# Optimization experiments

Measured on AMD Instinct MI355X. Metric: run time of the kernel, lower is better.

The kernel has to match this reference:

```python
import jax, jax.numpy as jnp
import numpy as np


def _softmax_bmm(sjt, x):
    # sjt: [b, m, n] scores; softmax over n, then weighted sum of x [b, n, d]
    a = jax.nn.softmax(sjt, axis=2)
    return jnp.einsum('bmn,bnd->bmd', a, x)


def concat_att(x, y, Wc1, Wc2, vc):
    s1 = x @ Wc1  # [b, n, h]
    s2 = y @ Wc2  # [b, m, h]
    sjt = jnp.tanh(s1[:, None, :, :] + s2[:, :, None, :]) @ vc  # [b, m, n]
    return _softmax_bmm(sjt, x)


def dot_att(x, y, Wd, vd):
    # torch: vd(tanh(Wd(x_n * y_m))) ; (x_n*y_m)@Wd == einsum over feature dim
    s = jnp.einsum('bnd,bmd,dh->bmnh', x, y, Wd)  # [b, m, n, h]
    sjt = jnp.tanh(s) @ vd  # [b, m, n]
    return _softmax_bmm(sjt, x)


def minus_att(x, y, Wm, vm):
    # (x_n - y_m)@Wm == x@Wm broadcast-minus y@Wm
    sx = x @ Wm  # [b, n, h]
    sy = y @ Wm  # [b, m, h]
    sjt = jnp.tanh(sx[:, None, :, :] - sy[:, :, None, :]) @ vm  # [b, m, n]
    return _softmax_bmm(sjt, x)


def bilinear_att(x, y, Wb):
    sjt = jnp.einsum('bmd,bnd->bmn', y, x @ Wb)
    return _softmax_bmm(sjt, x)


def setup_inputs() -> dict:
    H = 128          # hidden_size
    D = 2 * H        # encoder feature dim (2*hidden)
    B, N, M = 4, 256, 256
    key = jax.random.key(0)
    ks = jax.random.split(key, 12)
    sD = 1.0 / np.sqrt(D)
    sH = 1.0 / np.sqrt(H)
    return {
        'x0_enc': jax.random.normal(ks[0], (B, N, D), jnp.float32),
        'x1_enc': jax.random.normal(ks[1], (B, M, D), jnp.float32),
        'Wc1': jax.random.normal(ks[2], (D, H), jnp.float32) * sD,
        'Wc2': jax.random.normal(ks[3], (D, H), jnp.float32) * sD,
        'vc': jax.random.normal(ks[4], (H,), jnp.float32) * sH,
        'Wb': jax.random.normal(ks[5], (D, D), jnp.float32) * sD,
        'Wd1': jax.random.normal(ks[6], (D, H), jnp.float32) * sD,
        'vd1': jax.random.normal(ks[7], (H,), jnp.float32) * sH,
        'Wd2': jax.random.normal(ks[8], (D, H), jnp.float32) * sD,
        'vd2': jax.random.normal(ks[9], (H,), jnp.float32) * sH,
        'Wm': jax.random.normal(ks[10], (D, H), jnp.float32) * sD,
        'vm': jax.random.normal(ks[11], (H,), jnp.float32) * sH,
    }


def reference(x0_enc, x1_enc, Wc1, Wc2, vc, Wb, Wd1, vd1, Wd2, vd2, Wm, vm):
    # attention_type == 'all'
    qtc = concat_att(x0_enc, x1_enc, Wc1, Wc2, vc)   # [b, m, d]
    qtb = bilinear_att(x0_enc, x1_enc, Wb)           # [b, m, d]
    qts = dot_att(x0_enc, x1_enc, Wd1, vd1)          # [b, m, d]
    qtd = dot_att(x1_enc, x0_enc, Wd2, vd2)          # [b, n, d] (n == m)
    qtm = minus_att(x0_enc, x1_enc, Wm, vm)          # [b, m, d]
    stacked = jnp.stack([x1_enc, qts, qtc, qtd, qtb, qtm], axis=0)
    return jnp.max(stacked, axis=0)
```

## Files before the change

kernel.cpp:

```cpp
#include <hip/hip_runtime.h>
#include <math.h>

typedef short short8 __attribute__((ext_vector_type(8)));
typedef float f32x4 __attribute__((ext_vector_type(4)));
typedef unsigned short US;

#if __has_builtin(__builtin_amdgcn_exp2f)
#define EXP2(x) __builtin_amdgcn_exp2f(x)
#else
#define EXP2(x) exp2f(x)
#endif
#define RCP(x) __builtin_amdgcn_rcpf(x)

#define C2 2.8853900817779268f

__device__ __forceinline__ float bf2f(US u) {
    return __uint_as_float(((unsigned int)u) << 16);
}
__device__ __forceinline__ US f2bf(float f) {
    unsigned int x = __float_as_uint(f);
    return (US)((x + 0x7FFFu + ((x >> 16) & 1u)) >> 16);
}
__device__ __forceinline__ US f2bf_fast(float f) {
    return (US)((__float_as_uint(f) + 0x8000u) >> 16);
}


__global__ void prep_kernel(const float* __restrict__ x0, const float* __restrict__ x1,
                            const float* __restrict__ Wc1, const float* __restrict__ Wc2,
                            const float* __restrict__ Wm, const float* __restrict__ Wd1,
                            const float* __restrict__ Wd2, const float* __restrict__ Wb,
                            US* __restrict__ x0b, US* __restrict__ x1b,
                            US* __restrict__ x0lo, US* __restrict__ x1lo,
                            US* __restrict__ WcT1, US* __restrict__ WcT2,
                            US* __restrict__ WmT, US* __restrict__ WdT1, US* __restrict__ WdT2,
                            US* __restrict__ WbThi, US* __restrict__ WbTlo,
                            US* __restrict__ x0T, US* __restrict__ x1T) {
    const int id = blockIdx.x;
    const int t = threadIdx.x;
    if (id < 512) {
        const int tensor = id >> 8;
        const float* src = tensor ? x1 : x0;
        US* dhi = tensor ? x1b : x0b;
        US* dlo = tensor ? x1lo : x0lo;
        const int idx = (id & 255) * 256 + t;
        float4 v = ((const float4*)src)[idx];
        float f[4] = {v.x, v.y, v.z, v.w};
        ushort4 hi, lo;
        US* hp = (US*)&hi;
        US* lp = (US*)&lo;
        #pragma unroll
        for (int j = 0; j < 4; ++j) {
            US h = f2bf(f[j]);
            hp[j] = h;
            lp[j] = f2bf(f[j] - bf2f(h));
        }
        ((ushort4*)dhi)[idx] = hi;
        ((ushort4*)dlo)[idx] = lo;
    } else if (id < 1152) {
        const int j = id - 512;
        const int mat = j >> 7;
        const float* src = (mat == 0) ? Wc1 : (mat == 1) ? Wc2 : (mat == 2) ? Wm : (mat == 3) ? Wd1 : Wd2;
        US* dst = (mat == 0) ? WcT1 : (mat == 1) ? WcT2 : (mat == 2) ? WmT : (mat == 3) ? WdT1 : WdT2;
        const int el = (j & 127) * 256 + t;
        const int d = el >> 7, h = el & 127;
        dst[h * 256 + d] = f2bf(src[d * 128 + h]);
    } else if (id < 1408) {
        const int j = id - 1152;
        const int el = j * 256 + t;
        const int d = el >> 8, dp = el & 255;
        float v = Wb[d * 256 + dp];
        US h = f2bf(v);
        WbThi[dp * 256 + d] = h;
        WbTlo[dp * 256 + d] = f2bf(v - bf2f(h));
    } else {
        const int j = id - 1408;
        const int tensor = j >> 9;
        const int j2 = j & 511;
        const int b = j2 >> 7;
        const int dp = j2 & 127;
        const float* src = tensor ? x1 : x0;
        US* dst = tensor ? x1T : x0T;
        float2 v = *(const float2*)(src + (size_t)(b * 256 + t) * 256 + dp * 2);
        dst[(size_t)(b * 256 + dp * 2) * 256 + t] = f2bf(v.x);
        dst[(size_t)(b * 256 + dp * 2 + 1) * 256 + t] = f2bf(v.y);
    }
}

__global__ __launch_bounds__(512, 4)
void combo_kernel(const US* __restrict__ x0b, const US* __restrict__ x0lo,
                  const US* __restrict__ x1b,
                  const US* __restrict__ WcT1, const US* __restrict__ WcT2,
                  const US* __restrict__ WmT,
                  const US* __restrict__ WbThi, const US* __restrict__ WbTlo,
                  const US* __restrict__ WdT1, const US* __restrict__ WdT2,
                  const float* __restrict__ x0, const float* __restrict__ x1,
                  const float* __restrict__ vd1, const float* __restrict__ vd2,
                  US* __restrict__ S1T, US* __restrict__ SXT,
                  float* __restrict__ S2, float* __restrict__ SY,
                  US* __restrict__ XBhi, US* __restrict__ XBlo,
                  float* __restrict__ sjt_s, float* __restrict__ sjt_d) {
    __shared__ __align__(16) US Wp[128 * 256];
    const int bid = blockIdx.x;
    const int t = threadIdx.x;
    const int lane = t & 63;
    const int w = t >> 6;
    const int arow = lane & 15;
    const int kgrp = lane >> 4;

    if (bid < 192) {
        if (w >= 4) return;
        const int id = bid;
        const int rg = id & 15;
        const int t2 = id >> 4;
        const int b = t2 / 3;
        const int which = t2 - b * 3;

        const US* A = (which == 2 ? x1b : x0b) + (size_t)(b * 256 + rg * 16 + arow) * 256 + kgrp * 8;
        const US* Alo = x0lo + (size_t)(b * 256 + rg * 16 + arow) * 256 + kgrp * 8;

        const f32x4 vzero = {0.f, 0.f, 0.f, 0.f};
        f32x4 acc[4];
        #pragma unroll
        for (int cj = 0; cj < 4; ++cj) acc[cj] = vzero;

        if (which == 1) {
            #pragma unroll
            for (int kk = 0; kk < 8; ++kk) {
                short8 ahi = *(const short8*)(A + kk * 32);
                short8 alo = *(const short8*)(Alo + kk * 32);
                #pragma unroll
                for (int cj = 0; cj < 4; ++cj) {
                    const int ct = w * 4 + cj;
                    short8 bhi = *(const short8*)(WbThi + (ct * 16 + arow) * 256 + kk * 32 + kgrp * 8);
                    short8 blo = *(const short8*)(WbTlo + (ct * 16 + arow) * 256 + kk * 32 + kgrp * 8);
                    acc[cj] = __builtin_amdgcn_mfma_f32_16x16x32_bf16(ahi, bhi, acc[cj], 0, 0, 0);
                    acc[cj] = __builtin_amdgcn_mfma_f32_16x16x32_bf16(ahi, blo, acc[cj], 0, 0, 0);
                    acc[cj] = __builtin_amdgcn_mfma_f32_16x16x32_bf16(alo, bhi, acc[cj], 0, 0, 0);
                }
            }
            #pragma unroll
            for (int cj = 0; cj < 4; ++cj) {
                const int ct = w * 4 + cj;
                #pragma unroll
                for (int r = 0; r < 4; ++r) {
                    const int n = rg * 16 + kgrp * 4 + r;
                    const int dp = ct * 16 + arow;
                    float val = acc[cj][r];
                    US h = f2bf(val);
                    US l = f2bf(val - bf2f(h));
                    XBhi[(size_t)(b * 256 + n) * 256 + dp] = h;
                    XBlo[(size_t)(b * 256 + n) * 256 + dp] = l;
                }
            }
        } else {
            const US* WA = (which == 0) ? WcT1 : WcT2;
            #pragma unroll
            for (int kk = 0; kk < 8; ++kk) {
                short8 a = *(const short8*)(A + kk * 32);
                #pragma unroll
                for (int cj = 0; cj < 4; ++cj) {
                    const int ct = w * 4 + cj;
                    const US* brow = (ct < 8) ? (WA + (ct * 16 + arow) * 256)
                                              : (WmT + ((ct - 8) * 16 + arow) * 256);
                    short8 bf = *(const short8*)(brow + kk * 32 + kgrp * 8);
                    acc[cj] = __builtin_amdgcn_mfma_f32_16x16x32_bf16(a, bf, acc[cj], 0, 0, 0);
                }
            }
            #pragma unroll
            for (int cj = 0; cj < 4; ++cj) {
                const int ct = w * 4 + cj;
                #pragma unroll
                for (int r = 0; r < 4; ++r) {
                    const int row = rg * 16 + kgrp * 4 + r;
                    const int h = (ct < 8) ? ct * 16 + arow : (ct - 8) * 16 + arow;
                    float val = acc[cj][r];
                    if (which == 0) {
                        US* dst = (ct < 8) ? S1T : SXT;
                        dst[(size_t)(b * 256 + row) * 128 + h] = f2bf(val);
                    } else {
                        float* dst = (ct < 8) ? S2 : SY;
                        dst[(size_t)(b * 256 + row) * 128 + h] = val;
                    }
                }
            }
        }
        return;
    }

    const int id2 = bid - 192;
    const int m    = id2 & 255;
    const int b    = (id2 >> 8) & 3;
    const int mech = id2 >> 10;
    const US* xA = (mech == 0 ? x0b : x1b) + (size_t)b * 65536;
    const float* yrow = (mech == 0 ? x1 : x0) + (size_t)(b * 256 + m) * 256;
    const US* WT = (mech == 0 ? WdT1 : WdT2);
    const float* v = (mech == 0 ? vd1 : vd2);
    float* out = (mech == 0 ? sjt_s : sjt_d) + (size_t)(b * 256 + m) * 256;

    {
        const int dslot = t & 31;
        const int hset = t >> 5;
        float yv[8];
        float4 y0 = *(const float4*)(yrow + dslot * 8);
        float4 y1 = *(const float4*)(yrow + dslot * 8 + 4);
        yv[0] = y0.x * C2; yv[1] = y0.y * C2; yv[2] = y0.z * C2; yv[3] = y0.w * C2;
        yv[4] = y1.x * C2; yv[5] = y1.y * C2; yv[6] = y1.z * C2; yv[7] = y1.w * C2;
        #pragma unroll
        for (int k = 0; k < 8; ++k) {
            const int hq = hset * 8 + k;
            short8 wv = *(const short8*)(WT + (size_t)hq * 256 + dslot * 8);
            short8 ov;
            #pragma unroll
            for (int j = 0; j < 8; ++j)
                ov[j] = (short)f2bf_fast(bf2f((US)wv[j]) * yv[j]);
            *(short8*)(&Wp[hq * 256 + ((dslot ^ (hq & 15)) << 3)]) = ov;
        }
    }
    __syncthreads();

    float v2[8], vsum = 0.f;
    #pragma unroll
    for (int j = 0; j < 8; ++j) {
        const float vvv = v[j * 16 + arow];
        vsum += vvv;
        v2[j] = -2.0f * vvv;
    }

    const f32x4 vzero = {0.f, 0.f, 0.f, 0.f};
    f32x4 acc[2][8];
    #pragma unroll
    for (int i = 0; i < 2; ++i)
        #pragma unroll
        for (int j = 0; j < 8; ++j) acc[i][j] = vzero;

    __builtin_amdgcn_s_setprio(1);
    #pragma unroll
    for (int kk = 0; kk < 8; ++kk) {
        short8 af[2];
        #pragma unroll
        for (int i = 0; i < 2; ++i)
            af[i] = *(const short8*)(xA + (size_t)(w * 32 + i * 16 + arow) * 256 + kk * 32 + kgrp * 8);
        const int sl = ((kk * 4 + kgrp) ^ arow) << 3;
        #pragma unroll
        for (int j = 0; j < 8; ++j) {
            short8 bfr = *(const short8*)(&Wp[(j * 16 + arow) * 256 + sl]);
            #pragma unroll
            for (int i = 0; i < 2; ++i)
                acc[i][j] = __builtin_amdgcn_mfma_f32_16x16x32_bf16(af[i], bfr, acc[i][j], 0, 0, 0);
        }
    }
    __builtin_amdgcn_s_setprio(0);

    float pacc[2][4];
    #pragma unroll
    for (int i = 0; i < 2; ++i)
        #pragma unroll
        for (int r = 0; r < 4; ++r) pacc[i][r] = 0.f;
    #pragma unroll
    for (int j = 0; j < 8; ++j)
        #pragma unroll
        for (int i = 0; i < 2; ++i)
            #pragma unroll
            for (int r = 0; r < 4; ++r)
                pacc[i][r] = fmaf(v2[j], RCP(EXP2(acc[i][j][r]) + 1.0f), pacc[i][r]);

    #pragma unroll
    for (int i = 0; i < 2; ++i)
        #pragma unroll
        for (int r = 0; r < 4; ++r) {
            float pp = pacc[i][r] + vsum;
            pp += __shfl_xor(pp, 1);
            pp += __shfl_xor(pp, 2);
            pp += __shfl_xor(pp, 4);
            pp += __shfl_xor(pp, 8);
            if (arow == 0) out[w * 32 + i * 16 + kgrp * 4 + r] = pp;
        }
}

__global__ __launch_bounds__(256)
void bilinear_kernel(const US* __restrict__ x1b, const US* __restrict__ x1lo,
                     const US* __restrict__ XBhi, const US* __restrict__ XBlo,
                     float* __restrict__ sjt_b) {
    const int id = blockIdx.x;
    const int b = id >> 6;
    const int rem = id & 63;
    const int mt = rem >> 3;
    const int nq = rem & 7;
    const int t = threadIdx.x;
    const int lane = t & 63;
    const int w = t >> 6;
    const int arow = lane & 15;
    const int kgrp = lane >> 4;
    const int m0 = mt * 32 + (w & 1) * 16;
    const int nt = nq * 2 + (w >> 1);
    const size_t abase = (size_t)(b * 256 + m0 + arow) * 256 + kgrp * 8;
    const size_t bbase0 = (size_t)(b * 256 + nt * 16 + arow) * 256 + kgrp * 8;
    const f32x4 vzero = {0.f, 0.f, 0.f, 0.f};
    f32x4 acc = vzero;
    #pragma unroll
    for (int kk = 0; kk < 8; ++kk) {
        short8 ahi = *(const short8*)(x1b + abase + kk * 32);
        short8 alo = *(const short8*)(x1lo + abase + kk * 32);
        short8 bhi = *(const short8*)(XBhi + bbase0 + kk * 32);
        short8 blo = *(const short8*)(XBlo + bbase0 + kk * 32);
        acc = __builtin_amdgcn_mfma_f32_16x16x32_bf16(ahi, bhi, acc, 0, 0, 0);
        acc = __builtin_amdgcn_mfma_f32_16x16x32_bf16(ahi, blo, acc, 0, 0, 0);
        acc = __builtin_amdgcn_mfma_f32_16x16x32_bf16(alo, bhi, acc, 0, 0, 0);
    }
    float* outb = sjt_b + (size_t)b * 65536;
    #pragma unroll
    for (int r = 0; r < 4; ++r)
        outb[(size_t)(m0 + kgrp * 4 + r) * 256 + nt * 16 + arow] = acc[r];
}

__global__ void final_probs_kernel(const US* __restrict__ S1T, const US* __restrict__ SXT,
                                   const float* __restrict__ S2, const float* __restrict__ SY,
                                   const float* __restrict__ vc, const float* __restrict__ vm,
                                   const float* __restrict__ sjt_b,
                                   const float* __restrict__ sjt_s, const float* __restrict__ sjt_d,
                                   US* __restrict__ P) {
    __shared__ float srow[5][256];
    __shared__ float s2c[128], syc[128], vc2[128], vm2[128];
    __shared__ float vsums[2];
    const int id = blockIdx.x;
    const int b = id >> 8, m = id & 255;
    const int t = threadIdx.x;
    const size_t bm = (size_t)(b * 256 + m) * 256;

    if (t < 128) {
        s2c[t] = S2[(size_t)(b * 256 + m) * 128 + t] * C2;
        vc2[t] = -2.0f * vc[t];
    } else {
        const int h = t - 128;
        syc[h] = SY[(size_t)(b * 256 + m) * 128 + h] * C2;
        vm2[h] = -2.0f * vm[h];
    }
    if (t < 64) {
        float sv = vc[t] + vc[t + 64];
        #pragma unroll
        for (int off = 32; off >= 1; off >>= 1) sv += __shfl_xor(sv, off);
        if (t == 0) vsums[0] = sv;
    } else if (t < 128) {
        const int l = t - 64;
        float sv = vm[l] + vm[l + 64];
        #pragma unroll
        for (int off = 32; off >= 1; off >>= 1) sv += __shfl_xor(sv, off);
        if (l == 0) vsums[1] = sv;
    }
    __syncthreads();

    {
        const US* s1p = S1T + (size_t)(b * 256 + t) * 128;
        const US* sxp = SXT + (size_t)(b * 256 + t) * 128;
        float accC = 0.f, accM = 0.f;
        #pragma unroll 2
        for (int hb = 0; hb < 16; ++hb) {
            short8 s1v = *(const short8*)(s1p + hb * 8);
            short8 sxv = *(const short8*)(sxp + hb * 8);
            #pragma unroll
            for (int j = 0; j < 8; ++j) {
                const int h = hb * 8 + j;
                float s1 = bf2f((US)s1v[j]);
                float sx = bf2f((US)sxv[j]);
                float aC = fmaf(s1, C2, s2c[h]);
                float aM = fmaf(sx, C2, -syc[h]);
                accC = fmaf(vc2[h], RCP(EXP2(aC) + 1.0f), accC);
                accM = fmaf(vm2[h], RCP(EXP2(aM) + 1.0f), accM);
            }
        }
        srow[0][t] = accC + vsums[0];
        srow[1][t] = accM + vsums[1];
    }
    srow[2][t] = sjt_b[bm + t];
    srow[3][t] = sjt_s[bm + t];
    srow[4][t] = sjt_d[bm + t];
    __syncthreads();

    const int wv = t >> 6, lane = t & 63;
    for (int r = wv; r < 5; r += 4) {
        float v0 = srow[r][lane], v1 = srow[r][lane + 64];
        float v2 = srow[r][lane + 128], v3 = srow[r][lane + 192];
        float mx = fmaxf(fmaxf(v0, v1), fmaxf(v2, v3));
        #pragma unroll
        for (int off = 32; off >= 1; off >>= 1) mx = fmaxf(mx, __shfl_xor(mx, off));
        v0 = __expf(v0 - mx); v1 = __expf(v1 - mx);
        v2 = __expf(v2 - mx); v3 = __expf(v3 - mx);
        float s = v0 + v1 + v2 + v3;
        #pragma unroll
        for (int off = 32; off >= 1; off >>= 1) s += __shfl_xor(s, off);
        float inv = __fdividef(1.0f, s);
        srow[r][lane] = v0 * inv;       srow[r][lane + 64] = v1 * inv;
        srow[r][lane + 128] = v2 * inv; srow[r][lane + 192] = v3 * inv;
    }
    __syncthreads();

    #pragma unroll
    for (int r = 0; r < 5; ++r)
        P[(size_t)r * 262144 + bm + t] = f2bf(srow[r][t]);
}

__global__ __launch_bounds__(256)
void apply_kernel(const US* __restrict__ P, const US* __restrict__ x0T,
                  const US* __restrict__ x1T, const float* __restrict__ x1,
                  float* __restrict__ outp) {
    const int id = blockIdx.x;
    const int b = id >> 6;
    const int rem = id & 63;
    const int dt = rem >> 2;
    const int mq = rem & 3;
    const int t = threadIdx.x;
    const int lane = t & 63;
    const int w = t >> 6;
    const int arow = lane & 15;
    const int kgrp = lane >> 4;
    const int m0 = mq * 64 + w * 16;

    float vmax[4];
    #pragma unroll
    for (int r = 0; r < 4; ++r)
        vmax[r] = x1[(size_t)(b * 256 + m0 + kgrp * 4 + r) * 256 + dt * 16 + arow];

    const f32x4 vzero = {0.f, 0.f, 0.f, 0.f};
    #pragma unroll
    for (int mech = 0; mech < 5; ++mech) {
        const US* Bsrc = (mech == 4 ? x1T : x0T) + (size_t)(b * 256 + dt * 16 + arow) * 256;
        const US* Pm = P + (size_t)mech * 262144 + (size_t)(b * 256 + m0 + arow) * 256;
        f32x4 acc = vzero;
        #pragma unroll
        for (int kk = 0; kk < 8; ++kk) {
            short8 bf = *(const short8*)(Bsrc + kk * 32 + kgrp * 8);
            short8 af = *(const short8*)(Pm + kk * 32 + kgrp * 8);
            acc = __builtin_amdgcn_mfma_f32_16x16x32_bf16(af, bf, acc, 0, 0, 0);
        }
        #pragma unroll
        for (int r = 0; r < 4; ++r)
            vmax[r] = fmaxf(vmax[r], acc[r]);
    }

    #pragma unroll
    for (int r = 0; r < 4; ++r)
        outp[(size_t)(b * 256 + m0 + kgrp * 4 + r) * 256 + dt * 16 + arow] = vmax[r];
}

extern "C" void kernel_launch(void* const* d_in, const int* in_sizes, int n_in,
                              void* d_out, int out_size, void* d_ws, size_t ws_size,
                              hipStream_t stream) {
    (void)in_sizes; (void)n_in; (void)out_size; (void)ws_size;
    const float* x0  = (const float*)d_in[0];
    const float* x1  = (const float*)d_in[1];
    const float* Wc1 = (const float*)d_in[2];
    const float* Wc2 = (const float*)d_in[3];
    const float* vc  = (const float*)d_in[4];
    const float* Wb  = (const float*)d_in[5];
    const float* Wd1 = (const float*)d_in[6];
    const float* vd1 = (const float*)d_in[7];
    const float* Wd2 = (const float*)d_in[8];
    const float* vd2 = (const float*)d_in[9];
    const float* Wm  = (const float*)d_in[10];
    const float* vm  = (const float*)d_in[11];

    char* ws = (char*)d_ws;
    US*    x0b    = (US*)(ws + 0);
    US*    x1b    = (US*)(ws + 524288);
    US*    x0lo   = (US*)(ws + 1048576);
    US*    x1lo   = (US*)(ws + 1572864);
    US*    WcT1   = (US*)(ws + 2097152);
    US*    WcT2   = (US*)(ws + 2162688);
    US*    WmT    = (US*)(ws + 2228224);
    US*    WdT1   = (US*)(ws + 2293760);
    US*    WdT2   = (US*)(ws + 2359296);
    US*    WbThi  = (US*)(ws + 2424832);
    US*    WbTlo  = (US*)(ws + 2555904);
    US*    S1T    = (US*)(ws + 2686976);
    US*    SXT    = (US*)(ws + 2949120);
    float* S2     = (float*)(ws + 3211264);
    float* SY     = (float*)(ws + 3735552);
    US*    XBhi   = (US*)(ws + 4259840);
    US*    XBlo   = (US*)(ws + 4784128);
    US*    x0T    = (US*)(ws + 5308416);
    US*    x1T    = (US*)(ws + 5832704);
    float* sjt_b  = (float*)(ws + 6356992);
    float* sjt_s  = (float*)(ws + 7405568);
    float* sjt_d  = (float*)(ws + 8454144);
    US*    P      = (US*)(ws + 9502720);

    prep_kernel<<<2432, 256, 0, stream>>>(x0, x1, Wc1, Wc2, Wm, Wd1, Wd2, Wb,
                                          x0b, x1b, x0lo, x1lo,
                                          WcT1, WcT2, WmT, WdT1, WdT2, WbThi, WbTlo,
                                          x0T, x1T);
    combo_kernel<<<2240, 512, 0, stream>>>(x0b, x0lo, x1b, WcT1, WcT2, WmT, WbThi, WbTlo,
                                           WdT1, WdT2, x0, x1, vd1, vd2,
                                           S1T, SXT, S2, SY, XBhi, XBlo, sjt_s, sjt_d);
    bilinear_kernel<<<256, 256, 0, stream>>>(x1b, x1lo, XBhi, XBlo, sjt_b);
    final_probs_kernel<<<1024, 256, 0, stream>>>(S1T, SXT, S2, SY, vc, vm, sjt_b,
                                                 sjt_s, sjt_d, P);
    apply_kernel<<<256, 256, 0, stream>>>(P, x0T, x1T, x1, (float*)d_out);
}
```

Baseline: 98.43 us.

## Fold projection GEMMs into prep kernel and merge bilinear and tanh-score work into combo

The small projection GEMMs (x@Wc, x@Wm, x@Wb) move into the prep kernel, which now reads the fp32 inputs and weights directly and converts them to bf16 on the fly. This drops the separate weight transpose and pre-split passes. The bilinear score GEMM and the concat/minus tanh-score computation move into the big combo kernel as extra block types interleaved with the dot-attention blocks, which removes one launch and lets the work overlap. The final probability kernel now only reads precomputed scores. The trade-off is strided, uncoalesced fp32 weight reads inside the GEMM blocks, redundant conversions, and extra global round trips for the sjt_c and sjt_m buffers.

```diff
diff --git a/kernel.cpp b/kernel.cpp
--- a/kernel.cpp
+++ b/kernel.cpp
@@ -26,16 +26,17 @@
 }
 
 
-__global__ void prep_kernel(const float* __restrict__ x0, const float* __restrict__ x1,
-                            const float* __restrict__ Wc1, const float* __restrict__ Wc2,
-                            const float* __restrict__ Wm, const float* __restrict__ Wd1,
-                            const float* __restrict__ Wd2, const float* __restrict__ Wb,
-                            US* __restrict__ x0b, US* __restrict__ x1b,
-                            US* __restrict__ x0lo, US* __restrict__ x1lo,
-                            US* __restrict__ WcT1, US* __restrict__ WcT2,
-                            US* __restrict__ WmT, US* __restrict__ WdT1, US* __restrict__ WdT2,
-                            US* __restrict__ WbThi, US* __restrict__ WbTlo,
-                            US* __restrict__ x0T, US* __restrict__ x1T) {
+__global__ void prep_gemm_kernel(const float* __restrict__ x0, const float* __restrict__ x1,
+                                 const float* __restrict__ Wc1, const float* __restrict__ Wc2,
+                                 const float* __restrict__ Wm, const float* __restrict__ Wd1,
+                                 const float* __restrict__ Wd2, const float* __restrict__ Wb,
+                                 US* __restrict__ x0b, US* __restrict__ x1b,
+                                 US* __restrict__ x0lo, US* __restrict__ x1lo,
+                                 US* __restrict__ WdT1, US* __restrict__ WdT2,
+                                 US* __restrict__ x0T, US* __restrict__ x1T,
+                                 US* __restrict__ S1T, US* __restrict__ SXT,
+                                 float* __restrict__ S2, float* __restrict__ SY,
+                                 US* __restrict__ XBhi, US* __restrict__ XBlo) {
     const int id = blockIdx.x;
     const int t = threadIdx.x;
     if (id < 512) {
@@ -57,24 +58,20 @@
         }
         ((ushort4*)dhi)[idx] = hi;
         ((ushort4*)dlo)[idx] = lo;
-    } else if (id < 1152) {
+        return;
+    }
+    if (id < 768) {
         const int j = id - 512;
         const int mat = j >> 7;
-        const float* src = (mat == 0) ? Wc1 : (mat == 1) ? Wc2 : (mat == 2) ? Wm : (mat == 3) ? Wd1 : Wd2;
-        US* dst = (mat == 0) ? WcT1 : (mat == 1) ? WcT2 : (mat == 2) ? WmT : (mat == 3) ? WdT1 : WdT2;
+        const float* src = mat ? Wd2 : Wd1;
+        US* dst = mat ? WdT2 : WdT1;
         const int el = (j & 127) * 256 + t;
         const int d = el >> 7, h = el & 127;
         dst[h * 256 + d] = f2bf(src[d * 128 + h]);
-    } else if (id < 1408) {
-        const int j = id - 1152;
-        const int el = j * 256 + t;
-        const int d = el >> 8, dp = el & 255;
-        float v = Wb[d * 256 + dp];
-        US h = f2bf(v);
-        WbThi[dp * 256 + d] = h;
-        WbTlo[dp * 256 + d] = f2bf(v - bf2f(h));
-    } else {
-        const int j = id - 1408;
+        return;
+    }
+    if (id < 1792) {
+        const int j = id - 768;
         const int tensor = j >> 9;
         const int j2 = j & 511;
         const int b = j2 >> 7;
@@ -84,22 +81,123 @@
         float2 v = *(const float2*)(src + (size_t)(b * 256 + t) * 256 + dp * 2);
         dst[(size_t)(b * 256 + dp * 2) * 256 + t] = f2bf(v.x);
         dst[(size_t)(b * 256 + dp * 2 + 1) * 256 + t] = f2bf(v.y);
+        return;
+    }
+    const int gid = id - 1792;
+    const int rg = gid & 15;
+    const int t2 = gid >> 4;
+    const int b = t2 / 3;
+    const int which = t2 - b * 3;
+    const int lane = t & 63;
+    const int w = t >> 6;
+    const int arow = lane & 15;
+    const int kgrp = lane >> 4;
+
+    const float* Araw = ((which == 2) ? x1 : x0) + (size_t)(b * 256 + rg * 16 + arow) * 256 + kgrp * 8;
+
+    const f32x4 vzero = {0.f, 0.f, 0.f, 0.f};
+    f32x4 acc[4];
+    #pragma unroll
+    for (int cj = 0; cj < 4; ++cj) acc[cj] = vzero;
+
+    if (which == 1) {
+        #pragma unroll
+        for (int kk = 0; kk < 8; ++kk) {
+            float4 a0 = *(const float4*)(Araw + kk * 32);
+            float4 a1 = *(const float4*)(Araw + kk * 32 + 4);
+            float af[8] = {a0.x, a0.y, a0.z, a0.w, a1.x, a1.y, a1.z, a1.w};
+            short8 ahi, alo;
+            #pragma unroll
+            for (int j = 0; j < 8; ++j) {
+                US h = f2bf(af[j]);
+                ahi[j] = (short)h;
+                alo[j] = (short)f2bf(af[j] - bf2f(h));
+            }
+            #pragma unroll
+            for (int cj = 0; cj < 4; ++cj) {
+                const int ct = w * 4 + cj;
+                const int dp = ct * 16 + arow;
+                short8 bhi, blo;
+                #pragma unroll
+                for (int j = 0; j < 8; ++j) {
+                    float wv = Wb[(size_t)(kk * 32 + kgrp * 8 + j) * 256 + dp];
+                    US h = f2bf(wv);
+                    bhi[j] = (short)h;
+                    blo[j] = (short)f2bf(wv - bf2f(h));
+                }
+                acc[cj] = __builtin_amdgcn_mfma_f32_16x16x32_bf16(ahi, bhi, acc[cj], 0, 0, 0);
+                acc[cj] = __builtin_amdgcn_mfma_f32_16x16x32_bf16(ahi, blo, acc[cj], 0, 0, 0);
+                acc[cj] = __builtin_amdgcn_mfma_f32_16x16x32_bf16(alo, bhi, acc[cj], 0, 0, 0);
+            }
+        }
+        #pragma unroll
+        for (int cj = 0; cj < 4; ++cj) {
+            const int ct = w * 4 + cj;
+            #pragma unroll
+            for (int r = 0; r < 4; ++r) {
+                const int n = rg * 16 + kgrp * 4 + r;
+                const int dp = ct * 16 + arow;
+                float val = acc[cj][r];
+                US h = f2bf(val);
+                US l = f2bf(val - bf2f(h));
+                XBhi[(size_t)(b * 256 + n) * 256 + dp] = h;
+                XBlo[(size_t)(b * 256 + n) * 256 + dp] = l;
+            }
+        }
+    } else {
+        #pragma unroll
+        for (int kk = 0; kk < 8; ++kk) {
+            float4 a0 = *(const float4*)(Araw + kk * 32);
+            float4 a1 = *(const float4*)(Araw + kk * 32 + 4);
+            float af[8] = {a0.x, a0.y, a0.z, a0.w, a1.x, a1.y, a1.z, a1.w};
+            short8 a;
+            #pragma unroll
+            for (int j = 0; j < 8; ++j) a[j] = (short)f2bf(af[j]);
+            #pragma unroll
+            for (int cj = 0; cj < 4; ++cj) {
+                const int ct = w * 4 + cj;
+                const int h = (ct < 8) ? ct * 16 + arow : (ct - 8) * 16 + arow;
+                const float* Wsrc = (ct < 8) ? ((which == 0) ? Wc1 : Wc2) : Wm;
+                short8 bf;
+                #pragma unroll
+                for (int j = 0; j < 8; ++j)
+                    bf[j] = (short)f2bf(Wsrc[(size_t)(kk * 32 + kgrp * 8 + j) * 128 + h]);
+                acc[cj] = __builtin_amdgcn_mfma_f32_16x16x32_bf16(a, bf, acc[cj], 0, 0, 0);
+            }
+        }
+        #pragma unroll
+        for (int cj = 0; cj < 4; ++cj) {
+            const int ct = w * 4 + cj;
+            #pragma unroll
+            for (int r = 0; r < 4; ++r) {
+                const int row = rg * 16 + kgrp * 4 + r;
+                const int h = (ct < 8) ? ct * 16 + arow : (ct - 8) * 16 + arow;
+                float val = acc[cj][r];
+                if (which == 0) {
+                    US* dst = (ct < 8) ? S1T : SXT;
+                    dst[(size_t)(b * 256 + row) * 128 + h] = f2bf(val);
+                } else {
+                    float* dst = (ct < 8) ? S2 : SY;
+                    dst[(size_t)(b * 256 + row) * 128 + h] = val;
+                }
+            }
+        }
     }
 }
 
 __global__ __launch_bounds__(512, 4)
-void combo_kernel(const US* __restrict__ x0b, const US* __restrict__ x0lo,
-                  const US* __restrict__ x1b,
-                  const US* __restrict__ WcT1, const US* __restrict__ WcT2,
-                  const US* __restrict__ WmT,
-                  const US* __restrict__ WbThi, const US* __restrict__ WbTlo,
+void combo_kernel(const US* __restrict__ x0b, const US* __restrict__ x1b,
+                  const US* __restrict__ x1lo,
                   const US* __restrict__ WdT1, const US* __restrict__ WdT2,
                   const float* __restrict__ x0, const float* __restrict__ x1,
                   const float* __restrict__ vd1, const float* __restrict__ vd2,
-                  US* __restrict__ S1T, US* __restrict__ SXT,
-                  float* __restrict__ S2, float* __restrict__ SY,
-                  US* __restrict__ XBhi, US* __restrict__ XBlo,
-                  float* __restrict__ sjt_s, float* __restrict__ sjt_d) {
+                  const US* __restrict__ S1T, const US* __restrict__ SXT,
+                  const float* __restrict__ S2, const float* __restrict__ SY,
+                  const float* __restrict__ vc, const float* __restrict__ vm,
+                  const US* __restrict__ XBhi, const US* __restrict__ XBlo,
+                  float* __restrict__ sjt_s, float* __restrict__ sjt_d,
+                  float* __restrict__ sjt_c, float* __restrict__ sjt_m,
+                  float* __restrict__ sjt_b) {
     __shared__ __align__(16) US Wp[128 * 256];
     const int bid = blockIdx.x;
     const int t = threadIdx.x;
@@ -108,90 +206,93 @@
     const int arow = lane & 15;
     const int kgrp = lane >> 4;
 
-    if (bid < 192) {
-        if (w >= 4) return;
-        const int id = bid;
-        const int rg = id & 15;
-        const int t2 = id >> 4;
-        const int b = t2 / 3;
-        const int which = t2 - b * 3;
-
-        const US* A = (which == 2 ? x1b : x0b) + (size_t)(b * 256 + rg * 16 + arow) * 256 + kgrp * 8;
-        const US* Alo = x0lo + (size_t)(b * 256 + rg * 16 + arow) * 256 + kgrp * 8;
-
+    if (bid >= 3072) {
+        const int idx = bid - 3072;
+        const int b = idx >> 5;
+        const int rem = idx & 31;
+        const int mt = rem >> 2;
+        const int nq = rem & 3;
+        const int m0 = mt * 32 + (w & 1) * 16;
+        const int nt = nq * 4 + (w >> 1);
+        const size_t abase = (size_t)(b * 256 + m0 + arow) * 256 + kgrp * 8;
+        const size_t bbase0 = (size_t)(b * 256 + nt * 16 + arow) * 256 + kgrp * 8;
         const f32x4 vzero = {0.f, 0.f, 0.f, 0.f};
-        f32x4 acc[4];
-        #pragma unroll
-        for (int cj = 0; cj < 4; ++cj) acc[cj] = vzero;
-
-        if (which == 1) {
-            #pragma unroll
-            for (int kk = 0; kk < 8; ++kk) {
-                short8 ahi = *(const short8*)(A + kk * 32);
-                short8 alo = *(const short8*)(Alo + kk * 32);
-                #pragma unroll
-                for (int cj = 0; cj < 4; ++cj) {
-                    const int ct = w * 4 + cj;
-                    short8 bhi = *(const short8*)(WbThi + (ct * 16 + arow) * 256 + kk * 32 + kgrp * 8);
-                    short8 blo = *(const short8*)(WbTlo + (ct * 16 + arow) * 256 + kk * 32 + kgrp * 8);
-                    acc[cj] = __builtin_amdgcn_mfma_f32_16x16x32_bf16(ahi, bhi, acc[cj], 0, 0, 0);
-                    acc[cj] = __builtin_amdgcn_mfma_f32_16x16x32_bf16(ahi, blo, acc[cj], 0, 0, 0);
-                    acc[cj] = __builtin_amdgcn_mfma_f32_16x16x32_bf16(alo, bhi, acc[cj], 0, 0, 0);
-                }
+        f32x4 acc = vzero;
+        #pragma unroll
+        for (int kk = 0; kk < 8; ++kk) {
+            short8 ahi = *(const short8*)(x1b + abase + kk * 32);
+            short8 alo = *(const short8*)(x1lo + abase + kk * 32);
+            short8 bhi = *(const short8*)(XBhi + bbase0 + kk * 32);
+            short8 blo = *(const short8*)(XBlo + bbase0 + kk * 32);
+            acc = __builtin_amdgcn_mfma_f32_16x16x32_bf16(ahi, bhi, acc, 0, 0, 0);
+            acc = __builtin_amdgcn_mfma_f32_16x16x32_bf16(ahi, blo, acc, 0, 0, 0);
+            acc = __builtin_amdgcn_mfma_f32_16x16x32_bf16(alo, bhi, acc, 0, 0, 0);
+        }
+        float* outb = sjt_b + (size_t)b * 65536;
+        #pragma unroll
+        for (int r = 0; r < 4; ++r)
+            outb[(size_t)(m0 + kgrp * 4 + r) * 256 + nt * 16 + arow] = acc[r];
+        return;
+    }
+
+    const int q = bid / 3;
+    const int r3 = bid - q * 3;
+
+    if (r3 == 2) {
+        const int b = q >> 8, m = q & 255;
+        float* s2c  = (float*)Wp;
+        float* sycN = s2c + 128;
+        float* vc2l = sycN + 128;
+        float* vm2l = vc2l + 128;
+        float* vsums = vm2l + 128;
+
+        if (t < 128) {
+            s2c[t] = S2[(size_t)(b * 256 + m) * 128 + t] * C2;
+            vc2l[t] = -2.0f * vc[t];
+        } else if (t < 256) {
+            const int h = t - 128;
+            sycN[h] = -SY[(size_t)(b * 256 + m) * 128 + h] * C2;
+            vm2l[h] = -2.0f * vm[h];
+        } else if (t < 320) {
+            const int l = t - 256;
+            float sv = vc[l] + vc[l + 64];
+            #pragma unroll
+            for (int off = 32; off >= 1; off >>= 1) sv += __shfl_xor(sv, off);
+            if (l == 0) vsums[0] = sv;
+        } else if (t < 384) {
+            const int l = t - 320;
+            float sv = vm[l] + vm[l + 64];
+            #pragma unroll
+            for (int off = 32; off >= 1; off >>= 1) sv += __shfl_xor(sv, off);
+            if (l == 0) vsums[1] = sv;
+        }
+        __syncthreads();
+
+        const int half = t >> 8;
+        const int n = t & 255;
+        const US* sp = (half == 0 ? S1T : SXT) + (size_t)(b * 256 + n) * 128;
+        const float* scoef = half == 0 ? s2c : sycN;
+        const float* vco = half == 0 ? vc2l : vm2l;
+        float accv = 0.f;
+        #pragma unroll 2
+        for (int hb = 0; hb < 16; ++hb) {
+            short8 v8 = *(const short8*)(sp + hb * 8);
+            #pragma unroll
+            for (int j = 0; j < 8; ++j) {
+                const int h = hb * 8 + j;
+                float a = fmaf(bf2f((US)v8[j]), C2, scoef[h]);
+                accv = fmaf(vco[h], RCP(EXP2(a) + 1.0f), accv);
             }
-            #pragma unroll
-            for (int cj = 0; cj < 4; ++cj) {
-                const int ct = w * 4 + cj;
-                #pragma unroll
-                for (int r = 0; r < 4; ++r) {
-                    const int n = rg * 16 + kgrp * 4 + r;
-                    const int dp = ct * 16 + arow;
-                    float val = acc[cj][r];
-                    US h = f2bf(val);
-                    US l = f2bf(val - bf2f(h));
-                    XBhi[(size_t)(b * 256 + n) * 256 + dp] = h;
-                    XBlo[(size_t)(b * 256 + n) * 256 + dp] = l;
-                }
-            }
-        } else {
-            const US* WA = (which == 0) ? WcT1 : WcT2;
-            #pragma unroll
-            for (int kk = 0; kk < 8; ++kk) {
-                short8 a = *(const short8*)(A + kk * 32);
-                #pragma unroll
-                for (int cj = 0; cj < 4; ++cj) {
-                    const int ct = w * 4 + cj;
-                    const US* brow = (ct < 8) ? (WA + (ct * 16 + arow) * 256)
-                                              : (WmT + ((ct - 8) * 16 + arow) * 256);
-                    short8 bf = *(const short8*)(brow + kk * 32 + kgrp * 8);
-                    acc[cj] = __builtin_amdgcn_mfma_f32_16x16x32_bf16(a, bf, acc[cj], 0, 0, 0);
-                }
-            }
-            #pragma unroll
-            for (int cj = 0; cj < 4; ++cj) {
-                const int ct = w * 4 + cj;
-                #pragma unroll
-                for (int r = 0; r < 4; ++r) {
-                    const int row = rg * 16 + kgrp * 4 + r;
-                    const int h = (ct < 8) ? ct * 16 + arow : (ct - 8) * 16 + arow;
-                    float val = acc[cj][r];
-                    if (which == 0) {
-                        US* dst = (ct < 8) ? S1T : SXT;
-                        dst[(size_t)(b * 256 + row) * 128 + h] = f2bf(val);
-                    } else {
-                        float* dst = (ct < 8) ? S2 : SY;
-                        dst[(size_t)(b * 256 + row) * 128 + h] = val;
-                    }
-                }
-            }
-        }
+        }
+        float* dst = half == 0 ? sjt_c : sjt_m;
+        dst[(size_t)(b * 256 + m) * 256 + n] = accv + vsums[half];
         return;
     }
 
-    const int id2 = bid - 192;
-    const int m    = id2 & 255;
-    const int b    = (id2 >> 8) & 3;
-    const int mech = id2 >> 10;
+    const int idx = q * 2 + r3;
+    const int m    = idx & 255;
+    const int b    = (idx >> 8) & 3;
+    const int mech = idx >> 10;
     const US* xA = (mech == 0 ? x0b : x1b) + (size_t)b * 65536;
     const float* yrow = (mech == 0 ? x1 : x0) + (size_t)(b * 256 + m) * 256;
     const US* WT = (mech == 0 ? WdT1 : WdT2);
@@ -278,100 +379,18 @@
         }
 }
 
-__global__ __launch_bounds__(256)
-void bilinear_kernel(const US* __restrict__ x1b, const US* __restrict__ x1lo,
-                     const US* __restrict__ XBhi, const US* __restrict__ XBlo,
-                     float* __restrict__ sjt_b) {
-    const int id = blockIdx.x;
-    const int b = id >> 6;
-    const int rem = id & 63;
-    const int mt = rem >> 3;
-    const int nq = rem & 7;
-    const int t = threadIdx.x;
-    const int lane = t & 63;
-    const int w = t >> 6;
-    const int arow = lane & 15;
-    const int kgrp = lane >> 4;
-    const int m0 = mt * 32 + (w & 1) * 16;
-    const int nt = nq * 2 + (w >> 1);
-    const size_t abase = (size_t)(b * 256 + m0 + arow) * 256 + kgrp * 8;
-    const size_t bbase0 = (size_t)(b * 256 + nt * 16 + arow) * 256 + kgrp * 8;
-    const f32x4 vzero = {0.f, 0.f, 0.f, 0.f};
-    f32x4 acc = vzero;
-    #pragma unroll
-    for (int kk = 0; kk < 8; ++kk) {
-        short8 ahi = *(const short8*)(x1b + abase + kk * 32);
-        short8 alo = *(const short8*)(x1lo + abase + kk * 32);
-        short8 bhi = *(const short8*)(XBhi + bbase0 + kk * 32);
-        short8 blo = *(const short8*)(XBlo + bbase0 + kk * 32);
-        acc = __builtin_amdgcn_mfma_f32_16x16x32_bf16(ahi, bhi, acc, 0, 0, 0);
-        acc = __builtin_amdgcn_mfma_f32_16x16x32_bf16(ahi, blo, acc, 0, 0, 0);
-        acc = __builtin_amdgcn_mfma_f32_16x16x32_bf16(alo, bhi, acc, 0, 0, 0);
-    }
-    float* outb = sjt_b + (size_t)b * 65536;
-    #pragma unroll
-    for (int r = 0; r < 4; ++r)
-        outb[(size_t)(m0 + kgrp * 4 + r) * 256 + nt * 16 + arow] = acc[r];
-}
-
-__global__ void final_probs_kernel(const US* __restrict__ S1T, const US* __restrict__ SXT,
-                                   const float* __restrict__ S2, const float* __restrict__ SY,
-                                   const float* __restrict__ vc, const float* __restrict__ vm,
+__global__ void final_probs_kernel(const float* __restrict__ sjt_c, const float* __restrict__ sjt_m,
                                    const float* __restrict__ sjt_b,
                                    const float* __restrict__ sjt_s, const float* __restrict__ sjt_d,
                                    US* __restrict__ P) {
     __shared__ float srow[5][256];
-    __shared__ float s2c[128], syc[128], vc2[128], vm2[128];
-    __shared__ float vsums[2];
     const int id = blockIdx.x;
     const int b = id >> 8, m = id & 255;
     const int t = threadIdx.x;
     const size_t bm = (size_t)(b * 256 + m) * 256;
 
-    if (t < 128) {
-        s2c[t] = S2[(size_t)(b * 256 + m) * 128 + t] * C2;
-        vc2[t] = -2.0f * vc[t];
-    } else {
-        const int h = t - 128;
-        syc[h] = SY[(size_t)(b * 256 + m) * 128 + h] * C2;
-        vm2[h] = -2.0f * vm[h];
-    }
-    if (t < 64) {
-        float sv = vc[t] + vc[t + 64];
-        #pragma unroll
-        for (int off = 32; off >= 1; off >>= 1) sv += __shfl_xor(sv, off);
-        if (t == 0) vsums[0] = sv;
-    } else if (t < 128) {
-        const int l = t - 64;
-        float sv = vm[l] + vm[l + 64];
-        #pragma unroll
-        for (int off = 32; off >= 1; off >>= 1) sv += __shfl_xor(sv, off);
-        if (l == 0) vsums[1] = sv;
-    }
-    __syncthreads();
-
-    {
-        const US* s1p = S1T + (size_t)(b * 256 + t) * 128;
-        const US* sxp = SXT + (size_t)(b * 256 + t) * 128;
-        float accC = 0.f, accM = 0.f;
-        #pragma unroll 2
-        for (int hb = 0; hb < 16; ++hb) {
-            short8 s1v = *(const short8*)(s1p + hb * 8);
-            short8 sxv = *(const short8*)(sxp + hb * 8);
-            #pragma unroll
-            for (int j = 0; j < 8; ++j) {
-                const int h = hb * 8 + j;
-                float s1 = bf2f((US)s1v[j]);
-                float sx = bf2f((US)sxv[j]);
-                float aC = fmaf(s1, C2, s2c[h]);
-                float aM = fmaf(sx, C2, -syc[h]);
-                accC = fmaf(vc2[h], RCP(EXP2(aC) + 1.0f), accC);
-                accM = fmaf(vm2[h], RCP(EXP2(aM) + 1.0f), accM);
-            }
-        }
-        srow[0][t] = accC + vsums[0];
-        srow[1][t] = accM + vsums[1];
-    }
+    srow[0][t] = sjt_c[bm + t];
+    srow[1][t] = sjt_m[bm + t];
     srow[2][t] = sjt_b[bm + t];
     srow[3][t] = sjt_s[bm + t];
     srow[4][t] = sjt_d[bm + t];
@@ -465,35 +484,29 @@
     US*    x1b    = (US*)(ws + 524288);
     US*    x0lo   = (US*)(ws + 1048576);
     US*    x1lo   = (US*)(ws + 1572864);
-    US*    WcT1   = (US*)(ws + 2097152);
-    US*    WcT2   = (US*)(ws + 2162688);
-    US*    WmT    = (US*)(ws + 2228224);
-    US*    WdT1   = (US*)(ws + 2293760);
-    US*    WdT2   = (US*)(ws + 2359296);
-    US*    WbThi  = (US*)(ws + 2424832);
-    US*    WbTlo  = (US*)(ws + 2555904);
-    US*    S1T    = (US*)(ws + 2686976);
-    US*    SXT    = (US*)(ws + 2949120);
-    float* S2     = (float*)(ws + 3211264);
-    float* SY     = (float*)(ws + 3735552);
-    US*    XBhi   = (US*)(ws + 4259840);
-    US*    XBlo   = (US*)(ws + 4784128);
-    US*    x0T    = (US*)(ws + 5308416);
-    US*    x1T    = (US*)(ws + 5832704);
-    float* sjt_b  = (float*)(ws + 6356992);
-    float* sjt_s  = (float*)(ws + 7405568);
-    float* sjt_d  = (float*)(ws + 8454144);
-    US*    P      = (US*)(ws + 9502720);
-
-    prep_kernel<<<2432, 256, 0, stream>>>(x0, x1, Wc1, Wc2, Wm, Wd1, Wd2, Wb,
-                                          x0b, x1b, x0lo, x1lo,
-                                          WcT1, WcT2, WmT, WdT1, WdT2, WbThi, WbTlo,
-                                          x0T, x1T);
-    combo_kernel<<<2240, 512, 0, stream>>>(x0b, x0lo, x1b, WcT1, WcT2, WmT, WbThi, WbTlo,
-                                           WdT1, WdT2, x0, x1, vd1, vd2,
-                                           S1T, SXT, S2, SY, XBhi, XBlo, sjt_s, sjt_d);
-    bilinear_kernel<<<256, 256, 0, stream>>>(x1b, x1lo, XBhi, XBlo, sjt_b);
-    final_probs_kernel<<<1024, 256, 0, stream>>>(S1T, SXT, S2, SY, vc, vm, sjt_b,
-                                                 sjt_s, sjt_d, P);
+    US*    WdT1   = (US*)(ws + 2097152);
+    US*    WdT2   = (US*)(ws + 2162688);
+    US*    S1T    = (US*)(ws + 2228224);
+    US*    SXT    = (US*)(ws + 2490368);
+    float* S2     = (float*)(ws + 2752512);
+    float* SY     = (float*)(ws + 3276800);
+    US*    XBhi   = (US*)(ws + 3801088);
+    US*    XBlo   = (US*)(ws + 4325376);
+    US*    x0T    = (US*)(ws + 4849664);
+    US*    x1T    = (US*)(ws + 5373952);
+    float* sjt_b  = (float*)(ws + 5898240);
+    float* sjt_s  = (float*)(ws + 6946816);
+    float* sjt_d  = (float*)(ws + 7995392);
+    float* sjt_c  = (float*)(ws + 9043968);
+    float* sjt_m  = (float*)(ws + 10092544);
+    US*    P      = (US*)(ws + 11141120);
+
+    prep_gemm_kernel<<<1984, 256, 0, stream>>>(x0, x1, Wc1, Wc2, Wm, Wd1, Wd2, Wb,
+                                               x0b, x1b, x0lo, x1lo, WdT1, WdT2,
+                                               x0T, x1T, S1T, SXT, S2, SY, XBhi, XBlo);
+    combo_kernel<<<3200, 512, 0, stream>>>(x0b, x1b, x1lo, WdT1, WdT2, x0, x1, vd1, vd2,
+                                           S1T, SXT, S2, SY, vc, vm, XBhi, XBlo,
+                                           sjt_s, sjt_d, sjt_c, sjt_m, sjt_b);
+    final_probs_kernel<<<1024, 256, 0, stream>>>(sjt_c, sjt_m, sjt_b, sjt_s, sjt_d, P);
     apply_kernel<<<256, 256, 0, stream>>>(P, x0T, x1T, x1, (float*)d_out);
 }
```

Measured after the change: 102.0 us. +3.6%, slower.
